# Kernel tuning notes

Measured on AMD Instinct MI355X. Metric: run time of the kernel, lower is better.

## Reference

```python
import jax, jax.numpy as jnp
import numpy as np

N, E, F, EF, H = 10000, 320000, 512, 6, 256


def _lin(k, fan_in, fan_out):
    # torch.nn.Linear default init
    s = 1.0 / np.sqrt(fan_in)
    kw, kb = jax.random.split(k)
    W = jax.random.uniform(kw, (fan_in, fan_out), minval=-s, maxval=s, dtype=jnp.float32)
    b = jax.random.uniform(kb, (fan_out,), minval=-s, maxval=s, dtype=jnp.float32)
    return W, b


def setup_inputs() -> dict:
    key = jax.random.key(0)
    ks = jax.random.split(key, 13)
    inp = {}
    inp["x"] = jax.random.normal(ks[0], (N, F), dtype=jnp.float32)
    inp["edge_index"] = jax.random.randint(ks[1], (2, E), 0, N, dtype=jnp.int32)
    inp["edge_attr"] = jax.random.normal(ks[2], (E, EF), dtype=jnp.float32)
    shapes = {
        "We0a": (2 * F + EF, H), "We0b": (H, H),   # conv_in edge MLP
        "Wn0a": (F + H, H),      "Wn0b": (H, H),   # conv_in node MLP
        "We1a": (3 * H, H),      "We1b": (H, H),   # conv[0] edge MLP
        "Wn1a": (2 * H, H),      "Wn1b": (H, H),   # conv[0] node MLP
        "Wp1":  (H, H),          "Wp2":  (H, 1),   # EdgePredictorFromEdges
    }
    for i, (nm, (fi, fo)) in enumerate(shapes.items()):
        W, b = _lin(ks[3 + i % 10], fi, fo)
        inp[nm] = W
        inp["b" + nm[1:]] = b
    return inp


def _mp(x, src, dst, ea, Wea, bea, Web, beb, Wna, bna, Wnb, bnb, residual, agg_mean):
    # MetaLayer edge model: MLP(concat[x_i, x_j, edge_attr])
    e_in = jnp.concatenate([x[src], x[dst], ea], axis=-1)   # [E, ...]
    new_ea = jax.nn.relu(e_in @ Wea + bea) @ Web + beb
    if residual:
        new_ea = new_ea + ea
    # node model: aggregate incoming edges at dst, MLP(concat[x, agg])
    agg = jax.ops.segment_sum(new_ea, dst, num_segments=N)  # [N, H]
    if agg_mean:
        deg = jax.ops.segment_sum(jnp.ones((src.shape[0],), x.dtype), dst, num_segments=N)
        agg = agg / jnp.maximum(deg, 1.0)[:, None]
    n_in = jnp.concatenate([x, agg], axis=-1)
    new_x = jax.nn.relu(n_in @ Wna + bna) @ Wnb + bnb
    if residual:
        new_x = new_x + x
    return new_x, new_ea


def reference(x, edge_index, edge_attr,
              We0a, be0a, We0b, be0b, Wn0a, bn0a, Wn0b, bn0b,
              We1a, be1a, We1b, be1b, Wn1a, bn1a, Wn1b, bn1b,
              Wp1, bp1, Wp2, bp2):
    src, dst = edge_index[0], edge_index[1]
    # conv_in: dims change (F->H, EF->H) so no residual; base_aggregation='mean'
    x1, ea1 = _mp(x, src, dst, edge_attr, We0a, be0a, We0b, be0b,
                  Wn0a, bn0a, Wn0b, bn0b, residual=False, agg_mean=True)
    # conv[0]: dims match -> residual; default base_aggregation='sum'
    x2, ea2 = _mp(x1, src, dst, ea1, We1a, be1a, We1b, be1b,
                  Wn1a, bn1a, Wn1b, bn1b, residual=True, agg_mean=False)
    # EdgePredictorFromEdges (eval mode -> dropout is identity)
    h = jax.nn.leaky_relu(ea2 @ Wp1 + bp1)
    out = (h @ Wp2 + bp2)[:, 0]  # squeeze -> [E]
    return out
```

## Files before the change

kernel.cpp:

```cpp
#include <hip/hip_runtime.h>

#define N_NODES 10000
#define N_EDGES 320000
#define HD      256

typedef __attribute__((ext_vector_type(8))) short bf16x8;
typedef __attribute__((ext_vector_type(4))) float f32x4;
#define MFMA16 __builtin_amdgcn_mfma_f32_16x16x32_bf16

#define OFF_PD   2560000
#define OFF_BA   5120000
#define OFF_BB   7680000
#define OFF_BC   10240000
#define OFF_DEG  12800000
#define OFF_BCV  12810000
#define OFF_BAV  12810256
#define OFF_PW0  12810512

__device__ __forceinline__ ushort f2bf(float x) {
  union { float f; unsigned u; } c; c.f = x;
  unsigned r = (c.u + 0x7FFFu + ((c.u >> 16) & 1u)) >> 16;
  return (ushort)r;
}
__device__ __forceinline__ float bf2f(ushort h) {
  union { float f; unsigned u; } c; c.u = ((unsigned)h) << 16; return c.f;
}

__global__ __launch_bounds__(256)
void prep_split(const float* __restrict__ W, ushort* __restrict__ H,
                ushort* __restrict__ L)
{
  int slot = blockIdx.x * 256 + threadIdx.x;
  int s    = slot >> 10;
  int rem  = slot & 1023;
  int cf   = rem >> 6;
  int lane = rem & 63;
  int k0 = s * 32 + ((lane >> 4) << 3);
  int n  = cf * 16 + (lane & 15);
#pragma unroll
  for (int j = 0; j < 8; ++j) {
    float v = W[(k0 + j) * HD + n];
    ushort hi = f2bf(v);
    H[slot * 8 + j] = hi;
    L[slot * 8 + j] = f2bf(v - bf2f(hi));
  }
}

__global__ __launch_bounds__(256)
void node_gemm(const float* __restrict__ A1, int K1,
               const float* __restrict__ A2, int K2,
               const float* __restrict__ scale,
               const float* __restrict__ W,
               const float* __restrict__ bias,
               float* __restrict__ C, int M, int act)
{
  __shared__ float sA[64 * 36];
  __shared__ float sB[32 * 256];
  __shared__ float sBias[256];
  const int tid = threadIdx.x;
  const int r0  = blockIdx.x * 64;
  if (bias) sBias[tid] = bias[tid];
  const int ty = tid >> 4, tx = tid & 15;

  float acc[4][16];
#pragma unroll
  for (int r = 0; r < 4; r++)
#pragma unroll
    for (int c = 0; c < 16; c++) acc[r][c] = 0.f;

  const int K = K1 + K2;
  const int arow = tid >> 2;
  const int aks  = (tid & 3) * 8;
  const int gr_a = r0 + arow;

  for (int kb = 0; kb < K; kb += 32) {
    const float* Ap; int lda, koff; float sc = 1.0f;
    if (kb < K1) { Ap = A1; lda = K1; koff = kb; }
    else { Ap = A2; lda = K2; koff = kb - K1;
           if (scale) sc = scale[gr_a < M ? gr_a : M - 1]; }
#pragma unroll
    for (int j = 0; j < 8; j += 4) {
      float4 v;
      if (gr_a < M) v = *(const float4*)&Ap[(long)gr_a * lda + koff + aks + j];
      else { v.x = v.y = v.z = v.w = 0.f; }
      v.x *= sc; v.y *= sc; v.z *= sc; v.w *= sc;
      *(float4*)&sA[arow * 36 + aks + j] = v;
    }
#pragma unroll
    for (int j = 0; j < 8; j++) {
      int i = tid + 256 * j, row = i >> 6, c4 = i & 63;
      *(float4*)&sB[row * HD + c4 * 4] = *(const float4*)&W[(long)(kb + row) * HD + c4 * 4];
    }
    __syncthreads();
#pragma unroll 4
    for (int kk = 0; kk < 32; kk++) {
      float a0 = sA[(ty * 4 + 0) * 36 + kk];
      float a1 = sA[(ty * 4 + 1) * 36 + kk];
      float a2 = sA[(ty * 4 + 2) * 36 + kk];
      float a3 = sA[(ty * 4 + 3) * 36 + kk];
#pragma unroll
      for (int c = 0; c < 16; c++) {
        float b = sB[kk * HD + tx + 16 * c];
        acc[0][c] += a0 * b; acc[1][c] += a1 * b;
        acc[2][c] += a2 * b; acc[3][c] += a3 * b;
      }
    }
    __syncthreads();
  }

#pragma unroll
  for (int r = 0; r < 4; r++) {
    int gr = r0 + ty * 4 + r;
    if (gr >= M) continue;
#pragma unroll
    for (int c = 0; c < 16; c++) {
      int col = tx + 16 * c;
      float v = acc[r][c];
      if (bias) v += sBias[col];
      if (act)  v = fmaxf(v, 0.f);
      C[(long)gr * HD + col] = v;
    }
  }
}

__global__ __launch_bounds__(256)
void bias_fold_k(const float* __restrict__ v1, const float* __restrict__ v2,
                 const float* __restrict__ W, const float* __restrict__ base,
                 float* __restrict__ out)
{
  const int j = threadIdx.x;
  float s = base[j];
  for (int k = 0; k < HD; k++) {
    float v = v1[k] + (v2 ? v2[k] : 0.f);
    s += v * W[k * HD + j];
  }
  out[j] = s;
}

__global__ void rdeg_k(float* __restrict__ deg)
{
  int i = blockIdx.x * blockDim.x + threadIdx.x;
  if (i < N_NODES) deg[i] = 1.0f / fmaxf(deg[i], 1.0f);
}

__device__ __forceinline__ void build_h0(
    int tid, const float* __restrict__ Ps, const float* __restrict__ Pd,
    const float* sEA, const float* sW6, const float* sB0,
    const int* sSrc, const int* sDst, ushort* Ah, ushort* Al)
{
  const int el = tid >> 3, q = tid & 7;
  const int sv = sSrc[el], dv = sDst[el];
  float eav[6];
#pragma unroll
  for (int k = 0; k < 6; ++k) eav[k] = sEA[el * 6 + k];
  const float* ps = Ps + (long)sv * HD + q * 32;
  const float* pd = Pd + (long)dv * HD + q * 32;
  const int sw = (el & 7) << 4;
  char* ahB = (char*)Ah + el * 512;
  char* alB = (char*)Al + el * 512;
#pragma unroll
  for (int jj = 0; jj < 8; ++jj) {
    float4 a  = *(const float4*)(ps + jj * 4);
    float4 b  = *(const float4*)(pd + jj * 4);
    float4 bb = *(const float4*)(sB0 + q * 32 + jj * 4);
    float vx = a.x + b.x + bb.x;
    float vy = a.y + b.y + bb.y;
    float vz = a.z + b.z + bb.z;
    float vw = a.w + b.w + bb.w;
#pragma unroll
    for (int k = 0; k < 6; ++k) {
      float4 w = *(const float4*)(sW6 + k * HD + q * 32 + jj * 4);
      vx += eav[k] * w.x; vy += eav[k] * w.y;
      vz += eav[k] * w.z; vw += eav[k] * w.w;
    }
    vx = fmaxf(vx, 0.f); vy = fmaxf(vy, 0.f);
    vz = fmaxf(vz, 0.f); vw = fmaxf(vw, 0.f);
    ushort4 hh, ll;
    hh.x = f2bf(vx); hh.y = f2bf(vy); hh.z = f2bf(vz); hh.w = f2bf(vw);
    ll.x = f2bf(vx - bf2f(hh.x)); ll.y = f2bf(vy - bf2f(hh.y));
    ll.z = f2bf(vz - bf2f(hh.z)); ll.w = f2bf(vw - bf2f(hh.w));
    const int off = (q * 64 + jj * 8) ^ sw;
    *(ushort4*)(ahB + off) = hh;
    *(ushort4*)(alB + off) = ll;
  }
}

__device__ __forceinline__ void write_split(ushort* Ah, ushort* Al,
                                            int row, int col, float v)
{
  const int off = row * 512 + ((col * 2) ^ ((row & 7) << 4));
  ushort hi = f2bf(v);
  *(ushort*)((char*)Ah + off) = hi;
  *(ushort*)((char*)Al + off) = f2bf(v - bf2f(hi));
}

__device__ __forceinline__ void load_afrag(const ushort* Ah, const ushort* Al,
    int row, int s, int lane, bf16x8& ah, bf16x8& al)
{
  const int aoff = row * 512 + ((((s << 6) + ((lane >> 4) << 4))) ^ ((row & 7) << 4));
  ah = *(const bf16x8*)((const char*)Ah + aoff);
  al = *(const bf16x8*)((const char*)Al + aoff);
}

__global__ __launch_bounds__(512, 4)
void edge_conv_in(const int* __restrict__ ei, const float* __restrict__ eattr,
                  const float* __restrict__ Ps, const float* __restrict__ Pd,
                  const float* __restrict__ W6, const float* __restrict__ b0,
                  const ushort* __restrict__ pW0,
                  const float* __restrict__ be0b,
                  float* __restrict__ agg, float* __restrict__ deg)
{
  __shared__ ushort Ah[64 * 256];
  __shared__ ushort Al[64 * 256];
  __shared__ float  sW6[6 * 256];
  __shared__ float  sEA[64 * 6];
  __shared__ float  sB0[256];
  __shared__ int    sSrc[64], sDst[64];
  const int tid = threadIdx.x;
  const long e0 = (long)blockIdx.x * 64;

  if (tid < 64) {
    int dv = ei[N_EDGES + e0 + tid];
    sDst[tid] = dv;
    atomicAdd(&deg[dv], 1.0f);
  } else if (tid < 128) {
    sSrc[tid - 64] = ei[e0 + tid - 64];
  }
  if (tid < 96)  *(float4*)&sEA[tid * 4] = *(const float4*)&eattr[e0 * 6 + tid * 4];
  if (tid < 384) *(float4*)&sW6[tid * 4] = *(const float4*)&W6[tid * 4];
  if (tid < 64)  *(float4*)&sB0[tid * 4] = *(const float4*)&b0[tid * 4];
  __syncthreads();

  build_h0(tid, Ps, Pd, sEA, sW6, sB0, sSrc, sDst, Ah, Al);
  __syncthreads();

  const int lane = tid & 63, wid = tid >> 6;
  const int wc = wid & 3, wrg = wid >> 2;
  const bf16x8* pH = (const bf16x8*)pW0;
  const bf16x8* pL = (const bf16x8*)(pW0 + 65536);

  f32x4 acc[2][4];
#pragma unroll
  for (int rb = 0; rb < 2; ++rb)
#pragma unroll
    for (int cf = 0; cf < 4; ++cf) acc[rb][cf] = (f32x4){0.f, 0.f, 0.f, 0.f};

#pragma unroll 2
  for (int s = 0; s < 8; ++s) {
    bf16x8 ah[2], al[2];
#pragma unroll
    for (int rb = 0; rb < 2; ++rb)
      load_afrag(Ah, Al, (wrg * 2 + rb) * 16 + (lane & 15), s, lane, ah[rb], al[rb]);
#pragma unroll
    for (int cf = 0; cf < 4; ++cf) {
      const int slot = s * 1024 + (wc * 4 + cf) * 64 + lane;
      bf16x8 bh = pH[slot];
      bf16x8 bl = pL[slot];
#pragma unroll
      for (int rb = 0; rb < 2; ++rb) {
        acc[rb][cf] = MFMA16(al[rb], bh, acc[rb][cf], 0, 0, 0);
        acc[rb][cf] = MFMA16(ah[rb], bl, acc[rb][cf], 0, 0, 0);
        acc[rb][cf] = MFMA16(ah[rb], bh, acc[rb][cf], 0, 0, 0);
      }
    }
  }

#pragma unroll
  for (int rb = 0; rb < 2; ++rb) {
    const int rbase = (wrg * 2 + rb) * 16 + ((lane >> 4) << 2);
#pragma unroll
    for (int cf = 0; cf < 4; ++cf) {
      const int col = wc * 64 + cf * 16 + (lane & 15);
      const float bv = be0b[col];
#pragma unroll
      for (int r = 0; r < 4; ++r)
        atomicAdd(&agg[(long)sDst[rbase + r] * HD + col], acc[rb][cf][r] + bv);
    }
  }
}

__global__ __launch_bounds__(512, 4)
void edge_pred(const int* __restrict__ ei, const float* __restrict__ eattr,
               const float* __restrict__ Ps, const float* __restrict__ Pd,
               const float* __restrict__ W6, const float* __restrict__ b0,
               const float* __restrict__ P1s, const float* __restrict__ P1d,
               const ushort* __restrict__ pWA, const ushort* __restrict__ pWB,
               const ushort* __restrict__ pWc,
               const float* __restrict__ bA, const float* __restrict__ bc,
               const float* __restrict__ Wp2, const float* __restrict__ bp2,
               float* __restrict__ out)
{
  __shared__ ushort Ah[64 * 256];
  __shared__ ushort Al[64 * 256];
  __shared__ float  sW6[6 * 256];
  __shared__ float  sEA[64 * 6];
  __shared__ float  sB0[256];
  __shared__ float  sOut[64];
  __shared__ int    sSrc[64], sDst[64];
  const int tid = threadIdx.x;
  const long e0 = (long)blockIdx.x * 64;

  if (tid < 64) {
    sDst[tid] = ei[N_EDGES + e0 + tid];
    sOut[tid] = bp2[0];
  } else if (tid < 128) {
    sSrc[tid - 64] = ei[e0 + tid - 64];
  }
  if (tid < 96)  *(float4*)&sEA[tid * 4] = *(const float4*)&eattr[e0 * 6 + tid * 4];
  if (tid < 384) *(float4*)&sW6[tid * 4] = *(const float4*)&W6[tid * 4];
  if (tid < 64)  *(float4*)&sB0[tid * 4] = *(const float4*)&b0[tid * 4];
  __syncthreads();

  build_h0(tid, Ps, Pd, sEA, sW6, sB0, sSrc, sDst, Ah, Al);
  __syncthreads();

  const int lane = tid & 63, wid = tid >> 6;
  const int wc = wid & 3, wrg = wid >> 2;
  const bf16x8* pAH = (const bf16x8*)pWA;
  const bf16x8* pAL = (const bf16x8*)(pWA + 65536);
  const bf16x8* pBH = (const bf16x8*)pWB;
  const bf16x8* pBL = (const bf16x8*)(pWB + 65536);
  const bf16x8* pCH = (const bf16x8*)pWc;
  const bf16x8* pCL = (const bf16x8*)(pWc + 65536);

  f32x4 acc1[2][4], accT[2][4];
#pragma unroll
  for (int rb = 0; rb < 2; ++rb)
#pragma unroll
    for (int cf = 0; cf < 4; ++cf) {
      acc1[rb][cf] = (f32x4){0.f, 0.f, 0.f, 0.f};
      accT[rb][cf] = (f32x4){0.f, 0.f, 0.f, 0.f};
    }

#pragma unroll 2
  for (int s = 0; s < 8; ++s) {
    bf16x8 ah[2], al[2];
#pragma unroll
    for (int rb = 0; rb < 2; ++rb)
      load_afrag(Ah, Al, (wrg * 2 + rb) * 16 + (lane & 15), s, lane, ah[rb], al[rb]);
#pragma unroll
    for (int cf = 0; cf < 4; ++cf) {
      const int slot = s * 1024 + (wc * 4 + cf) * 64 + lane;
      bf16x8 b1h = pAH[slot];
      bf16x8 b1l = pAL[slot];
      bf16x8 b2h = pBH[slot];
      bf16x8 b2l = pBL[slot];
#pragma unroll
      for (int rb = 0; rb < 2; ++rb) {
        acc1[rb][cf] = MFMA16(al[rb], b1h, acc1[rb][cf], 0, 0, 0);
        acc1[rb][cf] = MFMA16(ah[rb], b1l, acc1[rb][cf], 0, 0, 0);
        acc1[rb][cf] = MFMA16(ah[rb], b1h, acc1[rb][cf], 0, 0, 0);
        accT[rb][cf] = MFMA16(al[rb], b2h, accT[rb][cf], 0, 0, 0);
        accT[rb][cf] = MFMA16(ah[rb], b2l, accT[rb][cf], 0, 0, 0);
        accT[rb][cf] = MFMA16(ah[rb], b2h, accT[rb][cf], 0, 0, 0);
      }
    }
  }
  __syncthreads();

#pragma unroll
  for (int rb = 0; rb < 2; ++rb) {
    const int rbase = (wrg * 2 + rb) * 16 + ((lane >> 4) << 2);
#pragma unroll
    for (int cf = 0; cf < 4; ++cf) {
      const int col = wc * 64 + cf * 16 + (lane & 15);
      const float bv = bA[col];
#pragma unroll
      for (int r = 0; r < 4; ++r) {
        const int row = rbase + r;
        float v = acc1[rb][cf][r] + P1s[(long)sSrc[row] * HD + col]
                                  + P1d[(long)sDst[row] * HD + col] + bv;
        write_split(Ah, Al, row, col, fmaxf(v, 0.f));
      }
    }
  }
  __syncthreads();

  f32x4 accZ[2][4];
#pragma unroll
  for (int rb = 0; rb < 2; ++rb)
#pragma unroll
    for (int cf = 0; cf < 4; ++cf) accZ[rb][cf] = (f32x4){0.f, 0.f, 0.f, 0.f};

#pragma unroll 2
  for (int s = 0; s < 8; ++s) {
    bf16x8 ah[2], al[2];
#pragma unroll
    for (int rb = 0; rb < 2; ++rb)
      load_afrag(Ah, Al, (wrg * 2 + rb) * 16 + (lane & 15), s, lane, ah[rb], al[rb]);
#pragma unroll
    for (int cf = 0; cf < 4; ++cf) {
      const int slot = s * 1024 + (wc * 4 + cf) * 64 + lane;
      bf16x8 bh = pCH[slot];
      bf16x8 bl = pCL[slot];
#pragma unroll
      for (int rb = 0; rb < 2; ++rb) {
        accZ[rb][cf] = MFMA16(al[rb], bh, accZ[rb][cf], 0, 0, 0);
        accZ[rb][cf] = MFMA16(ah[rb], bl, accZ[rb][cf], 0, 0, 0);
        accZ[rb][cf] = MFMA16(ah[rb], bh, accZ[rb][cf], 0, 0, 0);
      }
    }
  }

  float p[2][4] = {{0.f,0.f,0.f,0.f},{0.f,0.f,0.f,0.f}};
#pragma unroll
  for (int cf = 0; cf < 4; ++cf) {
    const int col = wc * 64 + cf * 16 + (lane & 15);
    const float w   = Wp2[col];
    const float bcv = bc[col];
#pragma unroll
    for (int rb = 0; rb < 2; ++rb)
#pragma unroll
      for (int r = 0; r < 4; ++r) {
        float z = accZ[rb][cf][r] + accT[rb][cf][r] + bcv;
        z = z > 0.f ? z : 0.01f * z;
        p[rb][r] += z * w;
      }
  }
#pragma unroll
  for (int rb = 0; rb < 2; ++rb)
#pragma unroll
    for (int r = 0; r < 4; ++r) {
      p[rb][r] += __shfl_xor(p[rb][r], 1);
      p[rb][r] += __shfl_xor(p[rb][r], 2);
      p[rb][r] += __shfl_xor(p[rb][r], 4);
      p[rb][r] += __shfl_xor(p[rb][r], 8);
    }
  if ((lane & 15) == 0) {
#pragma unroll
    for (int rb = 0; rb < 2; ++rb) {
      const int rbase = (wrg * 2 + rb) * 16 + ((lane >> 4) << 2);
#pragma unroll
      for (int r = 0; r < 4; ++r) atomicAdd(&sOut[rbase + r], p[rb][r]);
    }
  }
  __syncthreads();
  if (tid < 64) out[e0 + tid] = sOut[tid];
}

extern "C" void kernel_launch(void* const* d_in, const int* in_sizes, int n_in,
                              void* d_out, int out_size, void* d_ws, size_t ws_size,
                              hipStream_t stream)
{
  const float* x     = (const float*)d_in[0];
  const int*   ei    = (const int*)d_in[1];
  const float* eattr = (const float*)d_in[2];
  const float* We0a  = (const float*)d_in[3];
  const float* be0a  = (const float*)d_in[4];
  const float* We0b  = (const float*)d_in[5];
  const float* be0b  = (const float*)d_in[6];
  const float* Wn0a  = (const float*)d_in[7];
  const float* bn0a  = (const float*)d_in[8];
  const float* Wn0b  = (const float*)d_in[9];
  const float* bn0b  = (const float*)d_in[10];
  const float* We1a  = (const float*)d_in[11];
  const float* be1a  = (const float*)d_in[12];
  const float* We1b  = (const float*)d_in[13];
  const float* be1b  = (const float*)d_in[14];
  const float* Wp1   = (const float*)d_in[19];
  const float* bp1   = (const float*)d_in[20];
  const float* Wp2   = (const float*)d_in[21];
  const float* bp2   = (const float*)d_in[22];
  float* out = (float*)d_out;
  float* ws  = (float*)d_ws;

  float* P_s  = ws;
  float* P_d  = ws + OFF_PD;
  float* bufA = ws + OFF_BA;
  float* bufB = ws + OFF_BB;
  float* bufC = ws + OFF_BC;
  float* deg  = ws + OFF_DEG;
  float* bcB  = ws + OFF_BCV;
  float* bAB  = ws + OFF_BAV;
  ushort* pW0 = (ushort*)(ws + OFF_PW0);

  float*  WAf = ws + OFF_BB;
  float*  WBf = ws + OFF_BB + 65536;
  float*  WcF = ws + OFF_BB + 131072;
  ushort* pWA = (ushort*)(ws + OFF_BB + 196608);
  ushort* pWB = (ushort*)(ws + OFF_BB + 262144);
  ushort* pWc = (ushort*)(ws + OFF_BB + 327680);

  const float* W6  = We0a + 1024 * HD;
  const float* WeE = We1a + 512 * HD;

  hipMemsetAsync(bufC, 0, (2560000 + 10000) * sizeof(float), stream);

  const int ngrid = (N_NODES + 63) / 64;
  const int egrid = N_EDGES / 64;

  node_gemm<<<ngrid, 256, 0, stream>>>(x, 512, nullptr, 0, nullptr, We0a,            nullptr, P_s, N_NODES, 0);
  node_gemm<<<ngrid, 256, 0, stream>>>(x, 512, nullptr, 0, nullptr, We0a + 512 * HD, nullptr, P_d, N_NODES, 0);
  prep_split<<<32, 256, 0, stream>>>(We0b, pW0, pW0 + 65536);
  bias_fold_k<<<1, 256, 0, stream>>>(be1b, be0b, Wp1, bp1, bcB);
  bias_fold_k<<<1, 256, 0, stream>>>(be0b, nullptr, WeE, be1a, bAB);

  edge_conv_in<<<egrid, 512, 0, stream>>>(ei, eattr, P_s, P_d, W6, be0a,
                                          pW0, be0b, bufC, deg);
  rdeg_k<<<(N_NODES + 255) / 256, 256, 0, stream>>>(deg);

  node_gemm<<<ngrid, 256, 0, stream>>>(x, 512, bufC, 256, deg, Wn0a, bn0a, bufA, N_NODES, 1);
  node_gemm<<<ngrid, 256, 0, stream>>>(bufA, 256, nullptr, 0, nullptr, Wn0b, bn0b, bufB, N_NODES, 0);
  node_gemm<<<ngrid, 256, 0, stream>>>(bufB, 256, nullptr, 0, nullptr, We1a,            nullptr, bufA, N_NODES, 0);
  node_gemm<<<ngrid, 256, 0, stream>>>(bufB, 256, nullptr, 0, nullptr, We1a + 256 * HD, nullptr, bufC, N_NODES, 0);

  node_gemm<<<4, 256, 0, stream>>>(We0b, 256, nullptr, 0, nullptr, WeE, nullptr, WAf, 256, 0);
  node_gemm<<<4, 256, 0, stream>>>(We0b, 256, nullptr, 0, nullptr, Wp1, nullptr, WBf, 256, 0);
  node_gemm<<<4, 256, 0, stream>>>(We1b, 256, nullptr, 0, nullptr, Wp1, nullptr, WcF, 256, 0);
  prep_split<<<32, 256, 0, stream>>>(WAf, pWA, pWA + 65536);
  prep_split<<<32, 256, 0, stream>>>(WBf, pWB, pWB + 65536);
  prep_split<<<32, 256, 0, stream>>>(WcF, pWc, pWc + 65536);

  edge_pred<<<egrid, 512, 0, stream>>>(ei, eattr, P_s, P_d, W6, be0a,
      bufA, bufC, pWA, pWB, pWc, bAB, bcB, Wp2, bp2, out);
}
```

Before: 2.222 ms.

## Halve edge tile to 32 rows and drop shared staging of small weights

Measured after the change: 2.675 ms. 20.4% more time.

```diff
diff --git a/kernel.cpp b/kernel.cpp
--- a/kernel.cpp
+++ b/kernel.cpp
@@ -145,31 +145,33 @@
 
 __device__ __forceinline__ void build_h0(
     int tid, const float* __restrict__ Ps, const float* __restrict__ Pd,
-    const float* sEA, const float* sW6, const float* sB0,
+    const float* __restrict__ eattr, long e0,
+    const float* __restrict__ W6, const float* __restrict__ b0,
     const int* sSrc, const int* sDst, ushort* Ah, ushort* Al)
 {
-  const int el = tid >> 3, q = tid & 7;
+  const int el = tid >> 4, q = tid & 15;
   const int sv = sSrc[el], dv = sDst[el];
+  const long e = e0 + el;
   float eav[6];
 #pragma unroll
-  for (int k = 0; k < 6; ++k) eav[k] = sEA[el * 6 + k];
-  const float* ps = Ps + (long)sv * HD + q * 32;
-  const float* pd = Pd + (long)dv * HD + q * 32;
+  for (int k = 0; k < 6; ++k) eav[k] = eattr[e * 6 + k];
+  const float* ps = Ps + (long)sv * HD + q * 16;
+  const float* pd = Pd + (long)dv * HD + q * 16;
   const int sw = (el & 7) << 4;
   char* ahB = (char*)Ah + el * 512;
   char* alB = (char*)Al + el * 512;
 #pragma unroll
-  for (int jj = 0; jj < 8; ++jj) {
+  for (int jj = 0; jj < 4; ++jj) {
     float4 a  = *(const float4*)(ps + jj * 4);
     float4 b  = *(const float4*)(pd + jj * 4);
-    float4 bb = *(const float4*)(sB0 + q * 32 + jj * 4);
+    float4 bb = *(const float4*)(b0 + q * 16 + jj * 4);
     float vx = a.x + b.x + bb.x;
     float vy = a.y + b.y + bb.y;
     float vz = a.z + b.z + bb.z;
     float vw = a.w + b.w + bb.w;
 #pragma unroll
     for (int k = 0; k < 6; ++k) {
-      float4 w = *(const float4*)(sW6 + k * HD + q * 32 + jj * 4);
+      float4 w = *(const float4*)(W6 + k * HD + q * 16 + jj * 4);
       vx += eav[k] * w.x; vy += eav[k] * w.y;
       vz += eav[k] * w.z; vw += eav[k] * w.w;
     }
@@ -179,7 +181,7 @@
     hh.x = f2bf(vx); hh.y = f2bf(vy); hh.z = f2bf(vz); hh.w = f2bf(vw);
     ll.x = f2bf(vx - bf2f(hh.x)); ll.y = f2bf(vy - bf2f(hh.y));
     ll.z = f2bf(vz - bf2f(hh.z)); ll.w = f2bf(vw - bf2f(hh.w));
-    const int off = (q * 64 + jj * 8) ^ sw;
+    const int off = (q * 32 + jj * 8) ^ sw;
     *(ushort4*)(ahB + off) = hh;
     *(ushort4*)(alB + off) = ll;
   }
@@ -202,7 +204,30 @@
   al = *(const bf16x8*)((const char*)Al + aoff);
 }
 
-__global__ __launch_bounds__(512, 4)
+__device__ __forceinline__ void gemm_pass(
+    const ushort* __restrict__ pW,
+    const ushort* Ah, const ushort* Al,
+    int lane, int wc, int arow, f32x4 acc[4])
+{
+  const bf16x8* pH = (const bf16x8*)pW;
+  const bf16x8* pL = (const bf16x8*)(pW + 65536);
+#pragma unroll 2
+  for (int s = 0; s < 8; ++s) {
+    bf16x8 ah, al;
+    load_afrag(Ah, Al, arow, s, lane, ah, al);
+#pragma unroll
+    for (int cf = 0; cf < 4; ++cf) {
+      const int slot = s * 1024 + (wc * 4 + cf) * 64 + lane;
+      bf16x8 bh = pH[slot];
+      bf16x8 bl = pL[slot];
+      acc[cf] = MFMA16(al, bh, acc[cf], 0, 0, 0);
+      acc[cf] = MFMA16(ah, bl, acc[cf], 0, 0, 0);
+      acc[cf] = MFMA16(ah, bh, acc[cf], 0, 0, 0);
+    }
+  }
+}
+
+__global__ __launch_bounds__(512, 8)
 void edge_conv_in(const int* __restrict__ ei, const float* __restrict__ eattr,
                   const float* __restrict__ Ps, const float* __restrict__ Pd,
                   const float* __restrict__ W6, const float* __restrict__ b0,
@@ -210,76 +235,45 @@
                   const float* __restrict__ be0b,
                   float* __restrict__ agg, float* __restrict__ deg)
 {
-  __shared__ ushort Ah[64 * 256];
-  __shared__ ushort Al[64 * 256];
-  __shared__ float  sW6[6 * 256];
-  __shared__ float  sEA[64 * 6];
-  __shared__ float  sB0[256];
-  __shared__ int    sSrc[64], sDst[64];
+  __shared__ ushort Ah[32 * 256];
+  __shared__ ushort Al[32 * 256];
+  __shared__ int    sSrc[32], sDst[32];
   const int tid = threadIdx.x;
-  const long e0 = (long)blockIdx.x * 64;
-
-  if (tid < 64) {
+  const long e0 = (long)blockIdx.x * 32;
+
+  if (tid < 32) {
     int dv = ei[N_EDGES + e0 + tid];
     sDst[tid] = dv;
     atomicAdd(&deg[dv], 1.0f);
-  } else if (tid < 128) {
-    sSrc[tid - 64] = ei[e0 + tid - 64];
-  }
-  if (tid < 96)  *(float4*)&sEA[tid * 4] = *(const float4*)&eattr[e0 * 6 + tid * 4];
-  if (tid < 384) *(float4*)&sW6[tid * 4] = *(const float4*)&W6[tid * 4];
-  if (tid < 64)  *(float4*)&sB0[tid * 4] = *(const float4*)&b0[tid * 4];
-  __syncthreads();
-
-  build_h0(tid, Ps, Pd, sEA, sW6, sB0, sSrc, sDst, Ah, Al);
+  } else if (tid < 64) {
+    sSrc[tid - 32] = ei[e0 + tid - 32];
+  }
+  __syncthreads();
+
+  build_h0(tid, Ps, Pd, eattr, e0, W6, b0, sSrc, sDst, Ah, Al);
   __syncthreads();
 
   const int lane = tid & 63, wid = tid >> 6;
   const int wc = wid & 3, wrg = wid >> 2;
-  const bf16x8* pH = (const bf16x8*)pW0;
-  const bf16x8* pL = (const bf16x8*)(pW0 + 65536);
-
-  f32x4 acc[2][4];
-#pragma unroll
-  for (int rb = 0; rb < 2; ++rb)
-#pragma unroll
-    for (int cf = 0; cf < 4; ++cf) acc[rb][cf] = (f32x4){0.f, 0.f, 0.f, 0.f};
-
-#pragma unroll 2
-  for (int s = 0; s < 8; ++s) {
-    bf16x8 ah[2], al[2];
-#pragma unroll
-    for (int rb = 0; rb < 2; ++rb)
-      load_afrag(Ah, Al, (wrg * 2 + rb) * 16 + (lane & 15), s, lane, ah[rb], al[rb]);
-#pragma unroll
-    for (int cf = 0; cf < 4; ++cf) {
-      const int slot = s * 1024 + (wc * 4 + cf) * 64 + lane;
-      bf16x8 bh = pH[slot];
-      bf16x8 bl = pL[slot];
-#pragma unroll
-      for (int rb = 0; rb < 2; ++rb) {
-        acc[rb][cf] = MFMA16(al[rb], bh, acc[rb][cf], 0, 0, 0);
-        acc[rb][cf] = MFMA16(ah[rb], bl, acc[rb][cf], 0, 0, 0);
-        acc[rb][cf] = MFMA16(ah[rb], bh, acc[rb][cf], 0, 0, 0);
-      }
-    }
-  }
-
-#pragma unroll
-  for (int rb = 0; rb < 2; ++rb) {
-    const int rbase = (wrg * 2 + rb) * 16 + ((lane >> 4) << 2);
-#pragma unroll
-    for (int cf = 0; cf < 4; ++cf) {
-      const int col = wc * 64 + cf * 16 + (lane & 15);
-      const float bv = be0b[col];
-#pragma unroll
-      for (int r = 0; r < 4; ++r)
-        atomicAdd(&agg[(long)sDst[rbase + r] * HD + col], acc[rb][cf][r] + bv);
-    }
-  }
-}
-
-__global__ __launch_bounds__(512, 4)
+  const int arow = wrg * 16 + (lane & 15);
+
+  f32x4 acc[4];
+#pragma unroll
+  for (int cf = 0; cf < 4; ++cf) acc[cf] = (f32x4){0.f, 0.f, 0.f, 0.f};
+  gemm_pass(pW0, Ah, Al, lane, wc, arow, acc);
+
+  const int rbase = wrg * 16 + ((lane >> 4) << 2);
+#pragma unroll
+  for (int cf = 0; cf < 4; ++cf) {
+    const int col = wc * 64 + cf * 16 + (lane & 15);
+    const float bv = be0b[col];
+#pragma unroll
+    for (int r = 0; r < 4; ++r)
+      atomicAdd(&agg[(long)sDst[rbase + r] * HD + col], acc[cf][r] + bv);
+  }
+}
+
+__global__ __launch_bounds__(512, 8)
 void edge_pred(const int* __restrict__ ei, const float* __restrict__ eattr,
                const float* __restrict__ Ps, const float* __restrict__ Pd,
                const float* __restrict__ W6, const float* __restrict__ b0,
@@ -290,152 +284,85 @@
                const float* __restrict__ Wp2, const float* __restrict__ bp2,
                float* __restrict__ out)
 {
-  __shared__ ushort Ah[64 * 256];
-  __shared__ ushort Al[64 * 256];
-  __shared__ float  sW6[6 * 256];
-  __shared__ float  sEA[64 * 6];
-  __shared__ float  sB0[256];
-  __shared__ float  sOut[64];
-  __shared__ int    sSrc[64], sDst[64];
+  __shared__ ushort Ah[32 * 256];
+  __shared__ ushort Al[32 * 256];
+  __shared__ float  sOut[32];
+  __shared__ int    sSrc[32], sDst[32];
   const int tid = threadIdx.x;
-  const long e0 = (long)blockIdx.x * 64;
-
-  if (tid < 64) {
+  const long e0 = (long)blockIdx.x * 32;
+
+  if (tid < 32) {
     sDst[tid] = ei[N_EDGES + e0 + tid];
     sOut[tid] = bp2[0];
-  } else if (tid < 128) {
-    sSrc[tid - 64] = ei[e0 + tid - 64];
-  }
-  if (tid < 96)  *(float4*)&sEA[tid * 4] = *(const float4*)&eattr[e0 * 6 + tid * 4];
-  if (tid < 384) *(float4*)&sW6[tid * 4] = *(const float4*)&W6[tid * 4];
-  if (tid < 64)  *(float4*)&sB0[tid * 4] = *(const float4*)&b0[tid * 4];
-  __syncthreads();
-
-  build_h0(tid, Ps, Pd, sEA, sW6, sB0, sSrc, sDst, Ah, Al);
+  } else if (tid < 64) {
+    sSrc[tid - 32] = ei[e0 + tid - 32];
+  }
+  __syncthreads();
+
+  build_h0(tid, Ps, Pd, eattr, e0, W6, b0, sSrc, sDst, Ah, Al);
   __syncthreads();
 
   const int lane = tid & 63, wid = tid >> 6;
   const int wc = wid & 3, wrg = wid >> 2;
-  const bf16x8* pAH = (const bf16x8*)pWA;
-  const bf16x8* pAL = (const bf16x8*)(pWA + 65536);
-  const bf16x8* pBH = (const bf16x8*)pWB;
-  const bf16x8* pBL = (const bf16x8*)(pWB + 65536);
-  const bf16x8* pCH = (const bf16x8*)pWc;
-  const bf16x8* pCL = (const bf16x8*)(pWc + 65536);
-
-  f32x4 acc1[2][4], accT[2][4];
-#pragma unroll
-  for (int rb = 0; rb < 2; ++rb)
-#pragma unroll
-    for (int cf = 0; cf < 4; ++cf) {
-      acc1[rb][cf] = (f32x4){0.f, 0.f, 0.f, 0.f};
-      accT[rb][cf] = (f32x4){0.f, 0.f, 0.f, 0.f};
-    }
-
-#pragma unroll 2
-  for (int s = 0; s < 8; ++s) {
-    bf16x8 ah[2], al[2];
-#pragma unroll
-    for (int rb = 0; rb < 2; ++rb)
-      load_afrag(Ah, Al, (wrg * 2 + rb) * 16 + (lane & 15), s, lane, ah[rb], al[rb]);
-#pragma unroll
-    for (int cf = 0; cf < 4; ++cf) {
-      const int slot = s * 1024 + (wc * 4 + cf) * 64 + lane;
-      bf16x8 b1h = pAH[slot];
-      bf16x8 b1l = pAL[slot];
-      bf16x8 b2h = pBH[slot];
-      bf16x8 b2l = pBL[slot];
-#pragma unroll
-      for (int rb = 0; rb < 2; ++rb) {
-        acc1[rb][cf] = MFMA16(al[rb], b1h, acc1[rb][cf], 0, 0, 0);
-        acc1[rb][cf] = MFMA16(ah[rb], b1l, acc1[rb][cf], 0, 0, 0);
-        acc1[rb][cf] = MFMA16(ah[rb], b1h, acc1[rb][cf], 0, 0, 0);
-        accT[rb][cf] = MFMA16(al[rb], b2h, accT[rb][cf], 0, 0, 0);
-        accT[rb][cf] = MFMA16(ah[rb], b2l, accT[rb][cf], 0, 0, 0);
-        accT[rb][cf] = MFMA16(ah[rb], b2h, accT[rb][cf], 0, 0, 0);
-      }
-    }
-  }
-  __syncthreads();
-
-#pragma unroll
-  for (int rb = 0; rb < 2; ++rb) {
-    const int rbase = (wrg * 2 + rb) * 16 + ((lane >> 4) << 2);
-#pragma unroll
-    for (int cf = 0; cf < 4; ++cf) {
-      const int col = wc * 64 + cf * 16 + (lane & 15);
-      const float bv = bA[col];
-#pragma unroll
-      for (int r = 0; r < 4; ++r) {
-        const int row = rbase + r;
-        float v = acc1[rb][cf][r] + P1s[(long)sSrc[row] * HD + col]
-                                  + P1d[(long)sDst[row] * HD + col] + bv;
-        write_split(Ah, Al, row, col, fmaxf(v, 0.f));
-      }
-    }
-  }
-  __syncthreads();
-
-  f32x4 accZ[2][4];
-#pragma unroll
-  for (int rb = 0; rb < 2; ++rb)
-#pragma unroll
-    for (int cf = 0; cf < 4; ++cf) accZ[rb][cf] = (f32x4){0.f, 0.f, 0.f, 0.f};
-
-#pragma unroll 2
-  for (int s = 0; s < 8; ++s) {
-    bf16x8 ah[2], al[2];
-#pragma unroll
-    for (int rb = 0; rb < 2; ++rb)
-      load_afrag(Ah, Al, (wrg * 2 + rb) * 16 + (lane & 15), s, lane, ah[rb], al[rb]);
-#pragma unroll
-    for (int cf = 0; cf < 4; ++cf) {
-      const int slot = s * 1024 + (wc * 4 + cf) * 64 + lane;
-      bf16x8 bh = pCH[slot];
-      bf16x8 bl = pCL[slot];
-#pragma unroll
-      for (int rb = 0; rb < 2; ++rb) {
-        accZ[rb][cf] = MFMA16(al[rb], bh, accZ[rb][cf], 0, 0, 0);
-        accZ[rb][cf] = MFMA16(ah[rb], bl, accZ[rb][cf], 0, 0, 0);
-        accZ[rb][cf] = MFMA16(ah[rb], bh, accZ[rb][cf], 0, 0, 0);
-      }
-    }
-  }
-
-  float p[2][4] = {{0.f,0.f,0.f,0.f},{0.f,0.f,0.f,0.f}};
+  const int arow = wrg * 16 + (lane & 15);
+  const int rbase = wrg * 16 + ((lane >> 4) << 2);
+
+  f32x4 acc1[4];
+#pragma unroll
+  for (int cf = 0; cf < 4; ++cf) acc1[cf] = (f32x4){0.f, 0.f, 0.f, 0.f};
+  gemm_pass(pWA, Ah, Al, lane, wc, arow, acc1);
+
+  f32x4 accT[4];
+#pragma unroll
+  for (int cf = 0; cf < 4; ++cf) accT[cf] = (f32x4){0.f, 0.f, 0.f, 0.f};
+  gemm_pass(pWB, Ah, Al, lane, wc, arow, accT);
+  __syncthreads();
+
+#pragma unroll
+  for (int cf = 0; cf < 4; ++cf) {
+    const int col = wc * 64 + cf * 16 + (lane & 15);
+    const float bv = bA[col];
+#pragma unroll
+    for (int r = 0; r < 4; ++r) {
+      const int row = rbase + r;
+      float v = acc1[cf][r] + P1s[(long)sSrc[row] * HD + col]
+                            + P1d[(long)sDst[row] * HD + col] + bv;
+      write_split(Ah, Al, row, col, fmaxf(v, 0.f));
+    }
+  }
+  __syncthreads();
+
+  f32x4 accZ[4];
+#pragma unroll
+  for (int cf = 0; cf < 4; ++cf) accZ[cf] = (f32x4){0.f, 0.f, 0.f, 0.f};
+  gemm_pass(pWc, Ah, Al, lane, wc, arow, accZ);
+
+  float p[4] = {0.f, 0.f, 0.f, 0.f};
 #pragma unroll
   for (int cf = 0; cf < 4; ++cf) {
     const int col = wc * 64 + cf * 16 + (lane & 15);
     const float w   = Wp2[col];
     const float bcv = bc[col];
 #pragma unroll
-    for (int rb = 0; rb < 2; ++rb)
-#pragma unroll
-      for (int r = 0; r < 4; ++r) {
-        float z = accZ[rb][cf][r] + accT[rb][cf][r] + bcv;
-        z = z > 0.f ? z : 0.01f * z;
-        p[rb][r] += z * w;
-      }
-  }
-#pragma unroll
-  for (int rb = 0; rb < 2; ++rb)
-#pragma unroll
     for (int r = 0; r < 4; ++r) {
-      p[rb][r] += __shfl_xor(p[rb][r], 1);
-      p[rb][r] += __shfl_xor(p[rb][r], 2);
-      p[rb][r] += __shfl_xor(p[rb][r], 4);
-      p[rb][r] += __shfl_xor(p[rb][r], 8);
-    }
+      float z = accZ[cf][r] + accT[cf][r] + bcv;
+      z = z > 0.f ? z : 0.01f * z;
+      p[r] += z * w;
+    }
+  }
+#pragma unroll
+  for (int r = 0; r < 4; ++r) {
+    p[r] += __shfl_xor(p[r], 1);
+    p[r] += __shfl_xor(p[r], 2);
+    p[r] += __shfl_xor(p[r], 4);
+    p[r] += __shfl_xor(p[r], 8);
+  }
   if ((lane & 15) == 0) {
 #pragma unroll
-    for (int rb = 0; rb < 2; ++rb) {
-      const int rbase = (wrg * 2 + rb) * 16 + ((lane >> 4) << 2);
-#pragma unroll
-      for (int r = 0; r < 4; ++r) atomicAdd(&sOut[rbase + r], p[rb][r]);
-    }
-  }
-  __syncthreads();
-  if (tid < 64) out[e0 + tid] = sOut[tid];
+    for (int r = 0; r < 4; ++r) atomicAdd(&sOut[rbase + r], p[r]);
+  }
+  __syncthreads();
+  if (tid < 32) out[e0 + tid] = sOut[tid];
 }
 
 extern "C" void kernel_launch(void* const* d_in, const int* in_sizes, int n_in,
@@ -487,7 +414,7 @@
   hipMemsetAsync(bufC, 0, (2560000 + 10000) * sizeof(float), stream);
 
   const int ngrid = (N_NODES + 63) / 64;
-  const int egrid = N_EDGES / 64;
+  const int egrid = N_EDGES / 32;
 
   node_gemm<<<ngrid, 256, 0, stream>>>(x, 512, nullptr, 0, nullptr, We0a,            nullptr, P_s, N_NODES, 0);
   node_gemm<<<ngrid, 256, 0, stream>>>(x, 512, nullptr, 0, nullptr, We0a + 512 * HD, nullptr, P_d, N_NODES, 0);
```
